# Optimization experiments

Measured on AMD Instinct MI355X. Metric: run time of the kernel, lower is better.

The kernel has to match this reference:

```python
import jax, jax.numpy as jnp
import numpy as np

D_MODEL = 1024
NUM_HEADS = 16
D_K = D_MODEL // NUM_HEADS


def setup_inputs() -> dict:
    key = jax.random.key(0)
    ks = jax.random.split(key, 9)
    s = 1.0 / np.sqrt(D_MODEL)
    X = jax.random.normal(ks[0], (4, 2048, D_MODEL), dtype=jnp.float32)
    Wq = jax.random.uniform(ks[1], (D_MODEL, D_MODEL), jnp.float32, -s, s)
    bq = jax.random.uniform(ks[2], (D_MODEL,), jnp.float32, -s, s)
    Wk = jax.random.uniform(ks[3], (D_MODEL, D_MODEL), jnp.float32, -s, s)
    bk = jax.random.uniform(ks[4], (D_MODEL,), jnp.float32, -s, s)
    Wv = jax.random.uniform(ks[5], (D_MODEL, D_MODEL), jnp.float32, -s, s)
    bv = jax.random.uniform(ks[6], (D_MODEL,), jnp.float32, -s, s)
    Wo = jax.random.uniform(ks[7], (D_MODEL, D_MODEL), jnp.float32, -s, s)
    bo = jax.random.uniform(ks[8], (D_MODEL,), jnp.float32, -s, s)
    return {"X": X, "Wq": Wq, "bq": bq, "Wk": Wk, "bk": bk,
            "Wv": Wv, "bv": bv, "Wo": Wo, "bo": bo}


def reference(X, Wq, bq, Wk, bk, Wv, bv, Wo, bo):
    B, n, d = X.shape
    # Linear layers: y = x @ W^T + b (torch Linear convention)
    Q = X @ Wq.T + bq
    K = X @ Wk.T + bk
    V = X @ Wv.T + bv
    # [B, n, H, d_k] -> [B, H, n, d_k]
    Q = Q.reshape(B, n, NUM_HEADS, D_K).transpose(0, 2, 1, 3)
    K = K.reshape(B, n, NUM_HEADS, D_K).transpose(0, 2, 1, 3)
    V = V.reshape(B, n, NUM_HEADS, D_K).transpose(0, 2, 1, 3)
    scores = jnp.einsum('bhqd,bhkd->bhqk', Q, K) / jnp.sqrt(jnp.float32(D_K))
    attn = jax.nn.softmax(scores, axis=-1)  # [B, H, n, n]
    out = jnp.einsum('bhqk,bhkd->bhqd', attn, V)
    out = out.transpose(0, 2, 1, 3).reshape(B, n, d)
    return out @ Wo.T + bo
```

## Files before the change

kernel.cpp:

```cpp
#include <hip/hip_runtime.h>
#include <hip/hip_bf16.h>
#include <stdint.h>

typedef __hip_bfloat16 bf16;
typedef __bf16 bf16x8 __attribute__((ext_vector_type(8)));
typedef float floatx4 __attribute__((ext_vector_type(4)));

#define MFMA16(a, b, c) __builtin_amdgcn_mfma_f32_16x16x32_bf16((a), (b), (c), 0, 0, 0)

typedef __attribute__((address_space(3))) uint32_t lds_u32;
typedef const __attribute__((address_space(1))) uint32_t gbl_u32;

__device__ __forceinline__ void async16(const void* g, void* s) {
    __builtin_amdgcn_global_load_lds((gbl_u32*)g, (lds_u32*)s, 16, 0, 0);
}

__device__ __forceinline__ unsigned short f2bf_rne(float f) {
    union { float f; unsigned u; } v; v.f = f;
    const unsigned u = v.u;
    return (unsigned short)((u + 0x7FFFu + ((u >> 16) & 1u)) >> 16);
}
__device__ __forceinline__ unsigned pk2(float a, float b) {
    __hip_bfloat162 h = __float22bfloat162_rn(make_float2(a, b));
    return *(unsigned*)&h;
}

#define A_X   0L
#define A_WQ  8388608L
#define A_WK  9437184L
#define A_WV  10485760L
#define A_WO  11534336L
#define A_END 12582912L

__global__ __launch_bounds__(256) void cvt5(
    const float* __restrict__ s0, const float* __restrict__ s1,
    const float* __restrict__ s2, const float* __restrict__ s3,
    const float* __restrict__ s4, unsigned short* __restrict__ dst)
{
    const long beg[6] = {A_X, A_WQ, A_WK, A_WV, A_WO, A_END};
    const float* srcs[5] = {s0, s1, s2, s3, s4};
    const long nchunk = A_END / 8;
    for (long c = (long)blockIdx.x * 256 + threadIdx.x; c < nchunk;
         c += (long)gridDim.x * 256) {
        const long off = c * 8;
        int s = 0;
#pragma unroll
        for (int i = 1; i < 5; ++i) if (off >= beg[i]) s = i;
        const float* sp = srcs[s] + (off - beg[s]);
        const uint4 lo = *(const uint4*)(sp);
        const uint4 hi = *(const uint4*)(sp + 4);
        const float* fl = (const float*)&lo;
        const float* fh = (const float*)&hi;
        uint4 o;
        o.x = pk2(fl[0], fl[1]); o.y = pk2(fl[2], fl[3]);
        o.z = pk2(fh[0], fh[1]); o.w = pk2(fh[2], fh[3]);
        *(uint4*)(dst + off) = o;
    }
}

template <int CFP32, int TRANSV>
__global__ __launch_bounds__(256, 2) void gemm_bt3(
    const bf16* __restrict__ A,
    const bf16* __restrict__ W0, const bf16* __restrict__ W1, const bf16* __restrict__ W2,
    const float* __restrict__ b0, const float* __restrict__ b1, const float* __restrict__ b2,
    void* __restrict__ C0, void* __restrict__ C1, void* __restrict__ C2)
{
    __shared__ bf16 As[128 * 64];
    __shared__ bf16 Bs[128 * 64];

    const int tid = threadIdx.x;
    const int lin0 = blockIdx.y * 64 + blockIdx.x;
    const int nwg  = gridDim.y << 6;
    const int lin  = (lin0 & 7) * (nwg >> 3) + (lin0 >> 3);
    const int bx = lin & 63;
    const int by = lin >> 6;

    const int which = by >> 3;
    const int nt = by & 7;
    const bf16* __restrict__ W   = (which == 0) ? W0 : ((which == 1) ? W1 : W2);
    const float* __restrict__ bb = (which == 0) ? b0 : ((which == 1) ? b1 : b2);
    void* __restrict__ C         = (which == 0) ? C0 : ((which == 1) ? C1 : C2);

    const int m0 = bx * 128;
    const int n0 = nt * 128;

    const int w  = tid >> 6;
    const int l  = tid & 63;
    const int lr = l & 15;
    const int q  = l >> 4;
    const int wm = (w & 1) * 64;
    const int wn = (w >> 1) * 64;
    const int wbase = tid & 0xC0;

    floatx4 acc[4][4];
#pragma unroll
    for (int i = 0; i < 4; ++i)
#pragma unroll
        for (int j = 0; j < 4; ++j)
            acc[i][j] = (floatx4){0.f, 0.f, 0.f, 0.f};

#pragma unroll 1
    for (int kt = 0; kt < 16; ++kt) {
        __syncthreads();
#pragma unroll
        for (int r = 0; r < 4; ++r) {
            const int u   = r * 256 + tid;
            const int row = u >> 3;
            const int kg  = u & 7;
            const int kgg = kg ^ (row & 7);
            const size_t goffA = (size_t)(m0 + row) * 1024 + kt * 64 + kgg * 8;
            const size_t goffB = (size_t)(n0 + row) * 1024 + kt * 64 + kgg * 8;
            bf16* dA = As + (size_t)(r * 256 + wbase) * 8;
            bf16* dB = Bs + (size_t)(r * 256 + wbase) * 8;
            async16(A + goffA, dA);
            async16(W + goffB, dB);
        }
        asm volatile("s_waitcnt vmcnt(0)" ::: "memory");
        __syncthreads();

#pragma unroll
        for (int ks = 0; ks < 2; ++ks) {
            bf16x8 av[4], bv[4];
#pragma unroll
            for (int i = 0; i < 4; ++i) {
                const int row = wm + i * 16 + lr;
                const int kg  = (ks * 4 + q) ^ (row & 7);
                av[i] = *(const bf16x8*)(As + row * 64 + kg * 8);
            }
#pragma unroll
            for (int j = 0; j < 4; ++j) {
                const int row = wn + j * 16 + lr;
                const int kg  = (ks * 4 + q) ^ (row & 7);
                bv[j] = *(const bf16x8*)(Bs + row * 64 + kg * 8);
            }
#pragma unroll
            for (int i = 0; i < 4; ++i)
#pragma unroll
                for (int j = 0; j < 4; ++j)
                    acc[i][j] = MFMA16(av[i], bv[j], acc[i][j]);
        }
    }

    if (TRANSV && which == 2) {
#pragma unroll
        for (int j = 0; j < 4; ++j) {
            const int col = n0 + wn + j * 16 + lr;
            const float bj = bb[col];
            const int h = col >> 6, d = col & 63;
#pragma unroll
            for (int i = 0; i < 4; ++i) {
                const int row0 = m0 + wm + i * 16 + q * 4;
                const int b = row0 >> 11;
                const int key = row0 & 2047;
                uint2 ov;
                ov.x = pk2(acc[i][j][0] + bj, acc[i][j][1] + bj);
                ov.y = pk2(acc[i][j][2] + bj, acc[i][j][3] + bj);
                *(uint2*)((unsigned short*)C +
                          ((size_t)(b * 16 + h) * 64 + d) * 2048 + key) = ov;
            }
        }
    } else {
#pragma unroll
        for (int j = 0; j < 4; ++j) {
            const int col = n0 + wn + j * 16 + lr;
            const float bj = bb[col];
#pragma unroll
            for (int i = 0; i < 4; ++i) {
#pragma unroll
                for (int r = 0; r < 4; ++r) {
                    const int row = m0 + wm + i * 16 + q * 4 + r;
                    const float val = acc[i][j][r] + bj;
                    if (CFP32)
                        ((float*)C)[(long)row * 1024 + col] = val;
                    else
                        ((unsigned short*)C)[(long)row * 1024 + col] = f2bf_rne(val);
                }
            }
        }
    }
}

__device__ __forceinline__ int swzk(int R) {
    return (R & 7) ^ (((R >> 3) & 1) << 2);
}

__global__ __launch_bounds__(256, 2) void attn_flash(
    const bf16* __restrict__ Q, const bf16* __restrict__ K, const bf16* __restrict__ VT,
    bf16* __restrict__ AO)
{
    __shared__ bf16 Ks[2 * 64 * 64];
    __shared__ bf16 Vt[2 * 64 * 64];

    const int tid = threadIdx.x;
    const int b = blockIdx.y >> 4, h = blockIdx.y & 15;
    const int q0 = blockIdx.x * 128;
    const size_t base = ((size_t)b * 2048) * 1024 + (size_t)h * 64;
    const size_t vtb  = (size_t)(b * 16 + h) * 64 * 2048;

    const int w  = tid >> 6;
    const int l  = tid & 63;
    const int lr = l & 15;
    const int q  = l >> 4;

    const int srow = tid >> 3;
    const int soct = tid & 7;
    const int kr2  = 32 + srow;
    const int kg1  = soct ^ swzk(srow);
    const int kg2  = soct ^ swzk(kr2);
    const int vg1  = soct ^ (srow & 7);
    const int vg2  = soct ^ (kr2 & 7);
    const int wch  = (tid & 0xC0) * 8;

    bf16x8 qb[2][2];
#pragma unroll
    for (int i = 0; i < 2; ++i)
#pragma unroll
        for (int ks = 0; ks < 2; ++ks)
            qb[i][ks] = *(const bf16x8*)(Q + base +
                (size_t)(q0 + w * 32 + i * 16 + lr) * 1024 + ks * 32 + q * 8);

    {
        const bf16* kp = K + base;
        async16(kp + (size_t)srow * 1024 + kg1 * 8, Ks + wch);
        async16(kp + (size_t)kr2 * 1024 + kg2 * 8,  Ks + 2048 + wch);
        const bf16* vp = VT + vtb;
        async16(vp + (size_t)srow * 2048 + vg1 * 8, Vt + wch);
        async16(vp + (size_t)kr2 * 2048 + vg2 * 8,  Vt + 2048 + wch);
    }
    asm volatile("s_waitcnt vmcnt(0)" ::: "memory");
    __syncthreads();

    const floatx4 z4 = (floatx4){0.f, 0.f, 0.f, 0.f};
    floatx4 O0[4], O1[4];
#pragma unroll
    for (int d = 0; d < 4; ++d) { O0[d] = z4; O1[d] = z4; }
    float m0 = -1e30f, m1 = -1e30f;
    floatx4 ls0v = z4, ls1v = z4;
    const float cs = 0.18033688011112042f;

#pragma unroll 1
    for (int kt = 0; kt < 32; ++kt) {
        const int bsel = (kt & 1) * 4096;
        const int bnxt = 4096 - bsel;

        const int ktn = (kt < 31) ? (kt + 1) : 31;
        {
            const bf16* kp = K + base + (size_t)ktn * 65536;
            async16(kp + (size_t)srow * 1024 + kg1 * 8, Ks + bnxt + wch);
            async16(kp + (size_t)kr2 * 1024 + kg2 * 8,  Ks + bnxt + 2048 + wch);
            const bf16* vp = VT + vtb + (size_t)ktn * 64;
            async16(vp + (size_t)srow * 2048 + vg1 * 8, Vt + bnxt + wch);
            async16(vp + (size_t)kr2 * 2048 + vg2 * 8,  Vt + bnxt + 2048 + wch);
        }

        bf16x8 kb0[4], kb1[4];
#pragma unroll
        for (int t = 0; t < 4; ++t) {
            const int R = (t & 1) * 32 + (t >> 1) * 4 + (lr >> 2) * 8 + (lr & 3);
            kb0[t] = *(const bf16x8*)(Ks + bsel + R * 64 + ((q ^ swzk(R)) * 8));
            kb1[t] = *(const bf16x8*)(Ks + bsel + R * 64 + (((4 + q) ^ swzk(R)) * 8));
        }
        floatx4 s0[4], s1[4];
        __builtin_amdgcn_s_setprio(1);
#pragma unroll
        for (int t = 0; t < 4; ++t) s0[t] = MFMA16(kb0[t], qb[0][0], z4);
#pragma unroll
        for (int t = 0; t < 4; ++t) s0[t] = MFMA16(kb1[t], qb[0][1], s0[t]);
#pragma unroll
        for (int t = 0; t < 4; ++t) s1[t] = MFMA16(kb0[t], qb[1][0], z4);
#pragma unroll
        for (int t = 0; t < 4; ++t) s1[t] = MFMA16(kb1[t], qb[1][1], s1[t]);
        __builtin_amdgcn_s_setprio(0);

        float a0 = fmaxf(fmaxf(s0[0][0], s0[0][1]), s0[0][2]);
        float a1 = fmaxf(fmaxf(s0[0][3], s0[1][0]), s0[1][1]);
        float a2 = fmaxf(fmaxf(s0[1][2], s0[1][3]), s0[2][0]);
        float a3 = fmaxf(fmaxf(s0[2][1], s0[2][2]), s0[2][3]);
        float a4 = fmaxf(fmaxf(s0[3][0], s0[3][1]), s0[3][2]);
        const float mt0 = fmaxf(fmaxf(fmaxf(a0, a1), fmaxf(a2, a3)),
                                fmaxf(a4, s0[3][3])) * cs;
        float c0 = fmaxf(fmaxf(s1[0][0], s1[0][1]), s1[0][2]);
        float c1 = fmaxf(fmaxf(s1[0][3], s1[1][0]), s1[1][1]);
        float c2 = fmaxf(fmaxf(s1[1][2], s1[1][3]), s1[2][0]);
        float c3 = fmaxf(fmaxf(s1[2][1], s1[2][2]), s1[2][3]);
        float c4 = fmaxf(fmaxf(s1[3][0], s1[3][1]), s1[3][2]);
        const float mt1 = fmaxf(fmaxf(fmaxf(c0, c1), fmaxf(c2, c3)),
                                fmaxf(c4, s1[3][3])) * cs;

        if (__any((mt0 > m0 + 8.f) || (mt1 > m1 + 8.f))) {
            float vr0 = fmaxf(mt0, __shfl_xor(mt0, 16));
            vr0 = fmaxf(vr0, __shfl_xor(vr0, 32));
            const float mn0 = fmaxf(m0, vr0);
            const float al0 = __builtin_amdgcn_exp2f(m0 - mn0);
            m0 = mn0; ls0v *= al0;
#pragma unroll
            for (int d = 0; d < 4; ++d) O0[d] *= al0;
            float vr1 = fmaxf(mt1, __shfl_xor(mt1, 16));
            vr1 = fmaxf(vr1, __shfl_xor(vr1, 32));
            const float mn1 = fmaxf(m1, vr1);
            const float al1 = __builtin_amdgcn_exp2f(m1 - mn1);
            m1 = mn1; ls1v *= al1;
#pragma unroll
            for (int d = 0; d < 4; ++d) O1[d] *= al1;
        }

        bf16x8 va0[4];
#pragma unroll
        for (int dt = 0; dt < 4; ++dt) {
            const int R = dt * 16 + lr;
            va0[dt] = *(const bf16x8*)(Vt + bsel + R * 64 + ((q ^ (R & 7)) * 8));
        }

#pragma unroll
        for (int t = 0; t < 4; ++t)
#pragma unroll
            for (int r = 0; r < 4; ++r)
                s0[t][r] = __builtin_amdgcn_exp2f(s0[t][r] * cs - m0);
        ls0v += (s0[0] + s0[1]) + (s0[2] + s0[3]);
        bf16x8 pb0[2];
#pragma unroll
        for (int kc = 0; kc < 2; ++kc) {
            union { uint4 u; bf16x8 v; } pw;
            pw.u.x = pk2(s0[kc][0], s0[kc][1]);
            pw.u.y = pk2(s0[kc][2], s0[kc][3]);
            pw.u.z = pk2(s0[kc + 2][0], s0[kc + 2][1]);
            pw.u.w = pk2(s0[kc + 2][2], s0[kc + 2][3]);
            pb0[kc] = pw.v;
        }

        __builtin_amdgcn_s_setprio(1);
#pragma unroll
        for (int dt = 0; dt < 4; ++dt) O0[dt] = MFMA16(va0[dt], pb0[0], O0[dt]);
        __builtin_amdgcn_s_setprio(0);

        bf16x8 va1[4];
#pragma unroll
        for (int dt = 0; dt < 4; ++dt) {
            const int R = dt * 16 + lr;
            va1[dt] = *(const bf16x8*)(Vt + bsel + R * 64 +
                                       (((4 + q) ^ (R & 7)) * 8));
        }

#pragma unroll
        for (int t = 0; t < 4; ++t)
#pragma unroll
            for (int r = 0; r < 4; ++r)
                s1[t][r] = __builtin_amdgcn_exp2f(s1[t][r] * cs - m1);
        ls1v += (s1[0] + s1[1]) + (s1[2] + s1[3]);
        bf16x8 pb1[2];
#pragma unroll
        for (int kc = 0; kc < 2; ++kc) {
            union { uint4 u; bf16x8 v; } pw;
            pw.u.x = pk2(s1[kc][0], s1[kc][1]);
            pw.u.y = pk2(s1[kc][2], s1[kc][3]);
            pw.u.z = pk2(s1[kc + 2][0], s1[kc + 2][1]);
            pw.u.w = pk2(s1[kc + 2][2], s1[kc + 2][3]);
            pb1[kc] = pw.v;
        }

        __builtin_amdgcn_s_setprio(1);
#pragma unroll
        for (int dt = 0; dt < 4; ++dt) O0[dt] = MFMA16(va1[dt], pb0[1], O0[dt]);
#pragma unroll
        for (int dt = 0; dt < 4; ++dt) O1[dt] = MFMA16(va0[dt], pb1[0], O1[dt]);
#pragma unroll
        for (int dt = 0; dt < 4; ++dt) O1[dt] = MFMA16(va1[dt], pb1[1], O1[dt]);
        __builtin_amdgcn_s_setprio(0);

        asm volatile("s_waitcnt vmcnt(0)" ::: "memory");
        __syncthreads();
    }

    {
        float ls = (ls0v[0] + ls0v[1]) + (ls0v[2] + ls0v[3]);
        ls += __shfl_xor(ls, 16);
        ls += __shfl_xor(ls, 32);
        const float inv = 1.f / ls;
        const int row = q0 + w * 32 + lr;
#pragma unroll
        for (int dt = 0; dt < 4; ++dt) {
            uint2 oh;
            oh.x = pk2(O0[dt][0] * inv, O0[dt][1] * inv);
            oh.y = pk2(O0[dt][2] * inv, O0[dt][3] * inv);
            *(uint2*)((unsigned short*)AO + base + (size_t)row * 1024 +
                      dt * 16 + q * 4) = oh;
        }
    }
    {
        float ls = (ls1v[0] + ls1v[1]) + (ls1v[2] + ls1v[3]);
        ls += __shfl_xor(ls, 16);
        ls += __shfl_xor(ls, 32);
        const float inv = 1.f / ls;
        const int row = q0 + w * 32 + 16 + lr;
#pragma unroll
        for (int dt = 0; dt < 4; ++dt) {
            uint2 oh;
            oh.x = pk2(O1[dt][0] * inv, O1[dt][1] * inv);
            oh.y = pk2(O1[dt][2] * inv, O1[dt][3] * inv);
            *(uint2*)((unsigned short*)AO + base + (size_t)row * 1024 +
                      dt * 16 + q * 4) = oh;
        }
    }
}

extern "C" void kernel_launch(void* const* d_in, const int* in_sizes, int n_in,
                              void* d_out, int out_size, void* d_ws, size_t ws_size,
                              hipStream_t stream) {
    (void)in_sizes; (void)n_in; (void)out_size; (void)ws_size;
    const float* X  = (const float*)d_in[0];
    const float* Wq = (const float*)d_in[1];
    const float* bq = (const float*)d_in[2];
    const float* Wk = (const float*)d_in[3];
    const float* bk = (const float*)d_in[4];
    const float* Wv = (const float*)d_in[5];
    const float* bv = (const float*)d_in[6];
    const float* Wo = (const float*)d_in[7];
    const float* bo = (const float*)d_in[8];
    float* out = (float*)d_out;

    unsigned short* arena = (unsigned short*)d_ws;
    bf16* Xb  = (bf16*)(arena + A_X);
    bf16* Wqb = (bf16*)(arena + A_WQ);
    bf16* Wkb = (bf16*)(arena + A_WK);
    bf16* Wvb = (bf16*)(arena + A_WV);
    bf16* Wob = (bf16*)(arena + A_WO);

    const size_t SZ = (size_t)8192 * 1024;
    bf16* Qb  = (bf16*)(arena + A_END);
    bf16* Kb  = Qb + SZ;
    bf16* VTb = Kb + SZ;
    bf16* AOb = VTb + SZ;

    cvt5<<<dim3(1536), dim3(256), 0, stream>>>(X, Wq, Wk, Wv, Wo, arena);

    gemm_bt3<0, 1><<<dim3(64, 24), dim3(256), 0, stream>>>(
        Xb, Wqb, Wkb, Wvb, bq, bk, bv, (void*)Qb, (void*)Kb, (void*)VTb);

    attn_flash<<<dim3(16, 64), dim3(256), 0, stream>>>(Qb, Kb, VTb, AOb);

    gemm_bt3<1, 0><<<dim3(64, 8), dim3(256), 0, stream>>>(
        AOb, Wob, Wob, Wob, bo, bo, bo, (void*)out, (void*)out, (void*)out);
}
```

Before: 302.4 us.

## Enlarge attention blocks to 512 threads with register-staged K/V loads

The attention kernel now uses 512-thread blocks covering 256 query rows, so each K/V tile is shared by twice as many queries. K/V prefetch changes from async global-to-LDS loads to plain loads into registers, which are written to shared memory at the end of each iteration, with a single barrier at the top of the loop. The GEMM also drops its workgroup-index swizzle and uses the direct block mapping. The register staging adds VGPR pressure under a 512-thread, 4-block launch bound, and removing the swizzle may hurt L2 locality in the projections.

```diff
diff --git a/kernel.cpp b/kernel.cpp
--- a/kernel.cpp
+++ b/kernel.cpp
@@ -69,19 +69,13 @@
     __shared__ bf16 Bs[128 * 64];
 
     const int tid = threadIdx.x;
-    const int lin0 = blockIdx.y * 64 + blockIdx.x;
-    const int nwg  = gridDim.y << 6;
-    const int lin  = (lin0 & 7) * (nwg >> 3) + (lin0 >> 3);
-    const int bx = lin & 63;
-    const int by = lin >> 6;
-
-    const int which = by >> 3;
-    const int nt = by & 7;
+    const int which = blockIdx.y >> 3;
+    const int nt = blockIdx.y & 7;
     const bf16* __restrict__ W   = (which == 0) ? W0 : ((which == 1) ? W1 : W2);
     const float* __restrict__ bb = (which == 0) ? b0 : ((which == 1) ? b1 : b2);
     void* __restrict__ C         = (which == 0) ? C0 : ((which == 1) ? C1 : C2);
 
-    const int m0 = bx * 128;
+    const int m0 = blockIdx.x * 128;
     const int n0 = nt * 128;
 
     const int w  = tid >> 6;
@@ -184,7 +178,7 @@
     return (R & 7) ^ (((R >> 3) & 1) << 2);
 }
 
-__global__ __launch_bounds__(256, 2) void attn_flash(
+__global__ __launch_bounds__(512, 4) void attn_flash(
     const bf16* __restrict__ Q, const bf16* __restrict__ K, const bf16* __restrict__ VT,
     bf16* __restrict__ AO)
 {
@@ -193,7 +187,7 @@
 
     const int tid = threadIdx.x;
     const int b = blockIdx.y >> 4, h = blockIdx.y & 15;
-    const int q0 = blockIdx.x * 128;
+    const int q0 = blockIdx.x * 256;
     const size_t base = ((size_t)b * 2048) * 1024 + (size_t)h * 64;
     const size_t vtb  = (size_t)(b * 16 + h) * 64 * 2048;
 
@@ -204,12 +198,8 @@
 
     const int srow = tid >> 3;
     const int soct = tid & 7;
-    const int kr2  = 32 + srow;
-    const int kg1  = soct ^ swzk(srow);
-    const int kg2  = soct ^ swzk(kr2);
-    const int vg1  = soct ^ (srow & 7);
-    const int vg2  = soct ^ (kr2 & 7);
-    const int wch  = (tid & 0xC0) * 8;
+    const int stK = srow * 64 + ((soct ^ swzk(srow)) * 8);
+    const int stV = srow * 64 + ((soct ^ (srow & 7)) * 8);
 
     bf16x8 qb[2][2];
 #pragma unroll
@@ -219,16 +209,10 @@
             qb[i][ks] = *(const bf16x8*)(Q + base +
                 (size_t)(q0 + w * 32 + i * 16 + lr) * 1024 + ks * 32 + q * 8);
 
-    {
-        const bf16* kp = K + base;
-        async16(kp + (size_t)srow * 1024 + kg1 * 8, Ks + wch);
-        async16(kp + (size_t)kr2 * 1024 + kg2 * 8,  Ks + 2048 + wch);
-        const bf16* vp = VT + vtb;
-        async16(vp + (size_t)srow * 2048 + vg1 * 8, Vt + wch);
-        async16(vp + (size_t)kr2 * 2048 + vg2 * 8,  Vt + 2048 + wch);
-    }
-    asm volatile("s_waitcnt vmcnt(0)" ::: "memory");
-    __syncthreads();
+    uint4 kreg = *(const uint4*)(K + base + (size_t)srow * 1024 + soct * 8);
+    uint4 vreg = *(const uint4*)(VT + vtb + (size_t)srow * 2048 + soct * 8);
+    *(uint4*)(Ks + stK) = kreg;
+    *(uint4*)(Vt + stV) = vreg;
 
     const floatx4 z4 = (floatx4){0.f, 0.f, 0.f, 0.f};
     floatx4 O0[4], O1[4];
@@ -240,18 +224,15 @@
 
 #pragma unroll 1
     for (int kt = 0; kt < 32; ++kt) {
+        __syncthreads();
         const int bsel = (kt & 1) * 4096;
         const int bnxt = 4096 - bsel;
 
         const int ktn = (kt < 31) ? (kt + 1) : 31;
-        {
-            const bf16* kp = K + base + (size_t)ktn * 65536;
-            async16(kp + (size_t)srow * 1024 + kg1 * 8, Ks + bnxt + wch);
-            async16(kp + (size_t)kr2 * 1024 + kg2 * 8,  Ks + bnxt + 2048 + wch);
-            const bf16* vp = VT + vtb + (size_t)ktn * 64;
-            async16(vp + (size_t)srow * 2048 + vg1 * 8, Vt + bnxt + wch);
-            async16(vp + (size_t)kr2 * 2048 + vg2 * 8,  Vt + bnxt + 2048 + wch);
-        }
+        kreg = *(const uint4*)(K + base + (size_t)ktn * 65536 +
+                               (size_t)srow * 1024 + soct * 8);
+        vreg = *(const uint4*)(VT + vtb + (size_t)srow * 2048 +
+                               (size_t)ktn * 64 + soct * 8);
 
         bf16x8 kb0[4], kb1[4];
 #pragma unroll
@@ -367,8 +348,8 @@
         for (int dt = 0; dt < 4; ++dt) O1[dt] = MFMA16(va1[dt], pb1[1], O1[dt]);
         __builtin_amdgcn_s_setprio(0);
 
-        asm volatile("s_waitcnt vmcnt(0)" ::: "memory");
-        __syncthreads();
+        *(uint4*)(Ks + bnxt + stK) = kreg;
+        *(uint4*)(Vt + bnxt + stV) = vreg;
     }
 
     {
@@ -436,7 +417,7 @@
     gemm_bt3<0, 1><<<dim3(64, 24), dim3(256), 0, stream>>>(
         Xb, Wqb, Wkb, Wvb, bq, bk, bv, (void*)Qb, (void*)Kb, (void*)VTb);
 
-    attn_flash<<<dim3(16, 64), dim3(256), 0, stream>>>(Qb, Kb, VTb, AOb);
+    attn_flash<<<dim3(8, 64), dim3(512), 0, stream>>>(Qb, Kb, VTb, AOb);
 
     gemm_bt3<1, 0><<<dim3(64, 8), dim3(256), 0, stream>>>(
         AOb, Wob, Wob, Wob, bo, bo, bo, (void*)out, (void*)out, (void*)out);
```

New measurement: 305.4 us. Within noise of the previous version (+1.0%).
